# Kernel tuning notes

Hardware: AMD Instinct MI355X
Metric: run time of the kernel (lower is better)

Reference implementation:

```python
import jax, jax.numpy as jnp
import numpy as np

N = 100000      # nodes
E = 1600000     # edges (avg degree 16)
F_IN = 64
HID = 128
OUT = 64


def setup_inputs() -> dict:
    key = jax.random.key(0)
    ks = jax.random.split(key, 12)
    s = lambda k, i, o: jax.random.normal(k, (i, o), jnp.float32) / np.sqrt(i)
    x = jax.random.normal(ks[0], (N, F_IN), jnp.float32)
    edge_index = jax.random.randint(ks[1], (2, E), 0, N, dtype=jnp.int64)
    return {
        "x": x,
        "edge_index": edge_index,
        # conv1: SAGEConv(F_IN -> HID): lin_l (neighbors, with bias), lin_r (root)
        "W1n": s(ks[2], F_IN, HID), "b1n": jnp.zeros((HID,), jnp.float32),
        "W1r": s(ks[3], F_IN, HID),
        # lin1: Linear(F_IN -> HID)
        "Wl1": s(ks[4], F_IN, HID), "bl1": jnp.zeros((HID,), jnp.float32),
        # conv2: SAGEConv(HID -> OUT)
        "W2n": s(ks[5], HID, OUT), "b2n": jnp.zeros((OUT,), jnp.float32),
        "W2r": s(ks[6], HID, OUT),
        # lin2: Linear(HID -> OUT)
        "Wl2": s(ks[7], HID, OUT), "bl2": jnp.zeros((OUT,), jnp.float32),
    }


def _sage(x, src, dst, Wn, bn, Wr):
    # mean aggregation of source-node features at destination nodes
    msg = x[src]                                             # [E, F]
    agg = jax.ops.segment_sum(msg, dst, num_segments=N)      # [N, F]
    deg = jax.ops.segment_sum(jnp.ones((src.shape[0],), x.dtype), dst,
                              num_segments=N)                # [N]
    mean = agg / jnp.maximum(deg, 1.0)[:, None]
    return mean @ Wn + bn + x @ Wr


def reference(x, edge_index, W1n, b1n, W1r, Wl1, bl1, W2n, b2n, W2r, Wl2, bl2):
    src, dst = edge_index[0], edge_index[1]
    h = _sage(x, src, dst, W1n, b1n, W1r) + (x @ Wl1 + bl1)
    h = jax.nn.relu(h)
    out = _sage(h, src, dst, W2n, b2n, W2r) + (h @ Wl2 + bl2)
    return out
```

## Files before the change

kernel.cpp:

```cpp
#include <hip/hip_runtime.h>


#define NN 100000
#define NE 1600000
#define NSB 98
#define CAP2 18432
#define EPB 6250
#define MB 256
#define BSB 256
#define W1B 32
#define W2B 32
#define XBLK ((NN * 8 + 511) / 512)

typedef __attribute__((ext_vector_type(8))) __bf16 bf16x8;
typedef __attribute__((ext_vector_type(4))) float f32x4;

__device__ __forceinline__ float b2f(unsigned short u) {
    unsigned v = ((unsigned)u) << 16;
    float f;
    __builtin_memcpy(&f, &v, 4);
    return f;
}
__device__ __forceinline__ float b2f_lo(unsigned v) {
    unsigned w = v << 16;
    float f;
    __builtin_memcpy(&f, &w, 4);
    return f;
}
__device__ __forceinline__ float b2f_hi(unsigned v) {
    unsigned w = v & 0xFFFF0000u;
    float f;
    __builtin_memcpy(&f, &w, 4);
    return f;
}
__device__ __forceinline__ unsigned short f2b(float f) {
    unsigned u;
    __builtin_memcpy(&u, &f, 4);
    u += 0x7FFFu + ((u >> 16) & 1u);
    return (unsigned short)(u >> 16);
}

__global__ __launch_bounds__(512) void front_kernel(
    const void* __restrict__ x, const int* __restrict__ ei,
    const void* W1n, const void* W1r, const void* Wl1,
    const void* b1n, const void* bl1,
    const void* W2n, const void* W2r, const void* Wl2,
    const void* b2n, const void* bl2,
    unsigned short* __restrict__ Wt1g, unsigned short* __restrict__ Wt2g,
    float* __restrict__ bias1, float* __restrict__ bias2,
    unsigned int* __restrict__ xbu,
    int* __restrict__ flags, int* __restrict__ cntP, int* __restrict__ ebuf) {
    __shared__ int lh[NSB];
    __shared__ int lbase[NSB];
    __shared__ int ldst[EPB];
    __shared__ int sred[256];
    int t = threadIdx.x;
    int b = blockIdx.x;

    if (b < BSB) {
        if (t < 256) sred[t] = ei[2 * t + 1];
        if (t < NSB) lh[t] = 0;
        __syncthreads();
        for (int s = 128; s > 0; s >>= 1) {
            if (t < s) sred[t] |= sred[t + s];
            __syncthreads();
        }
        bool i64 = (sred[0] == 0);
        int e0 = b * EPB;
        for (int i = t; i < EPB; i += 512) {
            int e = e0 + i;
            int d = i64 ? (int)((const long long*)ei)[NE + e] : ei[NE + e];
            ldst[i] = d;
            atomicAdd(&lh[d >> 10], 1);
        }
        __syncthreads();
        if (t < NSB) {
            int c = lh[t];
            lbase[t] = c ? atomicAdd(&cntP[t * 16], c) : 0;
            lh[t] = 0;
        }
        __syncthreads();
        for (int i = t; i < EPB; i += 512) {
            int e = e0 + i;
            int s = i64 ? (int)((const long long*)ei)[e] : ei[e];
            int d = ldst[i];
            int sb = d >> 10;
            int r = lbase[sb] + atomicAdd(&lh[sb], 1);
            if (r < CAP2) ebuf[sb * CAP2 + r] = (s << 10) | (d & 1023);
        }
        return;
    }

    const unsigned int* xw = (const unsigned int*)x;
    if (t < 256) {
        unsigned e = (xw[t] >> 7) & 0xFFu;
        sred[t] = (e > 0x85u) ? 1 : 0;
    }
    __syncthreads();
    for (int s = 128; s > 0; s >>= 1) {
        if (t < s) sred[t] += sred[t + s];
        __syncthreads();
    }
    bool fp32 = sred[0] >= 32;
    auto rd = [&](const void* p, int i) -> float {
        return fp32 ? ((const float*)p)[i] : b2f(((const unsigned short*)p)[i]);
    };

    if (b < BSB + W1B) {
        int idx = (b - BSB) * 512 + t;
        int c = idx >> 7, k = idx & 127;
        float v = (k < 64) ? rd(W1n, k * 128 + c)
                           : rd(W1r, (k - 64) * 128 + c) + rd(Wl1, (k - 64) * 128 + c);
        Wt1g[c * 128 + k] = f2b(v);
        if (b == BSB) {
            if (t < 128) bias1[t] = rd(b1n, t) + rd(bl1, t);
            if (t == 0) flags[1] = fp32 ? 1 : 0;
        }
        return;
    }
    if (b < BSB + W1B + W2B) {
        int idx = (b - BSB - W1B) * 512 + t;
        int c = idx >> 7, k = idx & 127;
        float v = (c < 64) ? rd(W2n, k * 64 + c)
                           : rd(W2r, k * 64 + (c - 64)) + rd(Wl2, k * 64 + (c - 64));
        Wt2g[c * 128 + k] = f2b(v);
        if (b == BSB + W1B && t < 64) bias2[t] = rd(b2n, t) + rd(bl2, t);
        return;
    }
    int tt = (b - BSB - W1B - W2B) * 512 + t;
    if (tt >= NN * 8) return;
    if (fp32) {
        const float4* xf = (const float4*)x;
        float4 a = xf[2 * tt], c = xf[2 * tt + 1];
        uint4 o;
        o.x = f2b(a.x) | ((unsigned)f2b(a.y) << 16);
        o.y = f2b(a.z) | ((unsigned)f2b(a.w) << 16);
        o.z = f2b(c.x) | ((unsigned)f2b(c.y) << 16);
        o.w = f2b(c.z) | ((unsigned)f2b(c.w) << 16);
        ((uint4*)xbu)[tt] = o;
    } else {
        ((uint4*)xbu)[tt] = ((const uint4*)x)[tt];
    }
}

__global__ __launch_bounds__(512) void csr_build_kernel(
    const int* __restrict__ ebuf, const int* __restrict__ cntP,
    int* __restrict__ rpack, int* __restrict__ csr) {
    __shared__ int lcnt[1024];
    __shared__ int lsum[512];
    __shared__ int lcur[1024];
    int t = threadIdx.x, b = blockIdx.x;
    lcnt[t] = 0; lcnt[t + 512] = 0;
    __syncthreads();
    int base = b * CAP2;
    int cnt = min(cntP[b * 16], CAP2);
    for (int i = t; i < cnt; i += 512) atomicAdd(&lcnt[ebuf[base + i] & 1023], 1);
    __syncthreads();
    int c0 = lcnt[2 * t], c1 = lcnt[2 * t + 1];
    lsum[t] = c0 + c1;
    __syncthreads();
    for (int off = 1; off < 512; off <<= 1) {
        int v = lsum[t];
        int add = (t >= off) ? lsum[t - off] : 0;
        __syncthreads();
        lsum[t] = v + add;
        __syncthreads();
    }
    int excl = (t == 0) ? 0 : lsum[t - 1];
    int ex0 = excl, ex1 = excl + c0;
    lcur[2 * t] = ex0; lcur[2 * t + 1] = ex1;
    int d0 = b * 1024 + 2 * t;
    if (d0 < NN)     rpack[d0]     = ((base + ex0) << 8) | min(c0, 255);
    if (d0 + 1 < NN) rpack[d0 + 1] = ((base + ex1) << 8) | min(c1, 255);
    __syncthreads();
    for (int i = t; i < cnt; i += 512) {
        int pk = ebuf[base + i];
        int r = atomicAdd(&lcur[pk & 1023], 1);
        csr[base + r] = pk >> 10;
    }
}


__device__ __forceinline__ void gather_acc(
    const unsigned short* __restrict__ feat, const int* __restrict__ csr,
    int base, int deg, int fo, float* acc) {
    int t = 0;
    for (; t + 8 <= deg; t += 8) {
        int i0 = csr[base + t],     i1 = csr[base + t + 1];
        int i2 = csr[base + t + 2], i3 = csr[base + t + 3];
        int i4 = csr[base + t + 4], i5 = csr[base + t + 5];
        int i6 = csr[base + t + 6], i7 = csr[base + t + 7];
        bf16x8 v0 = *(const bf16x8*)(feat + (size_t)i0 * 64 + fo);
        bf16x8 v1 = *(const bf16x8*)(feat + (size_t)i1 * 64 + fo);
        bf16x8 v2 = *(const bf16x8*)(feat + (size_t)i2 * 64 + fo);
        bf16x8 v3 = *(const bf16x8*)(feat + (size_t)i3 * 64 + fo);
        bf16x8 v4 = *(const bf16x8*)(feat + (size_t)i4 * 64 + fo);
        bf16x8 v5 = *(const bf16x8*)(feat + (size_t)i5 * 64 + fo);
        bf16x8 v6 = *(const bf16x8*)(feat + (size_t)i6 * 64 + fo);
        bf16x8 v7 = *(const bf16x8*)(feat + (size_t)i7 * 64 + fo);
#pragma unroll
        for (int k = 0; k < 8; ++k)
            acc[k] += (((float)v0[k] + (float)v1[k]) + ((float)v2[k] + (float)v3[k]))
                    + (((float)v4[k] + (float)v5[k]) + ((float)v6[k] + (float)v7[k]));
    }
    for (; t + 4 <= deg; t += 4) {
        int i0 = csr[base + t],     i1 = csr[base + t + 1];
        int i2 = csr[base + t + 2], i3 = csr[base + t + 3];
        bf16x8 v0 = *(const bf16x8*)(feat + (size_t)i0 * 64 + fo);
        bf16x8 v1 = *(const bf16x8*)(feat + (size_t)i1 * 64 + fo);
        bf16x8 v2 = *(const bf16x8*)(feat + (size_t)i2 * 64 + fo);
        bf16x8 v3 = *(const bf16x8*)(feat + (size_t)i3 * 64 + fo);
#pragma unroll
        for (int k = 0; k < 8; ++k)
            acc[k] += ((float)v0[k] + (float)v1[k]) + ((float)v2[k] + (float)v3[k]);
    }
    for (; t < deg; ++t) {
        int i = csr[base + t];
        bf16x8 v = *(const bf16x8*)(feat + (size_t)i * 64 + fo);
#pragma unroll
        for (int k = 0; k < 8; ++k) acc[k] += (float)v[k];
    }
}

__global__ __launch_bounds__(256) void agg1_kernel(
    const unsigned short* __restrict__ feat, const int* __restrict__ rpack,
    const int* __restrict__ csr, unsigned int* __restrict__ mean1u) {
    int wid = threadIdx.x >> 6, lane = threadIdx.x & 63;
    int slot = lane >> 3, fo = (lane & 7) * 8;
    int d = (blockIdx.x * 4 + wid) * 8 + slot;
    int dd = min(d, NN - 1);
    int rp = rpack[dd];
    int base = rp >> 8;
    int deg = rp & 255;
    float acc[8];
#pragma unroll
    for (int k = 0; k < 8; ++k) acc[k] = 0.f;
    gather_acc(feat, csr, base, deg, fo, acc);
    if (d < NN) {
        float r = 1.0f / fmaxf((float)deg, 1.0f);
        uint4 o;
        o.x = f2b(acc[0] * r) | ((unsigned)f2b(acc[1] * r) << 16);
        o.y = f2b(acc[2] * r) | ((unsigned)f2b(acc[3] * r) << 16);
        o.z = f2b(acc[4] * r) | ((unsigned)f2b(acc[5] * r) << 16);
        o.w = f2b(acc[6] * r) | ((unsigned)f2b(acc[7] * r) << 16);
        *(uint4*)(mean1u + (size_t)d * 32 + (lane & 7) * 4) = o;
    }
}

__global__ __launch_bounds__(256) void agg2_kernel(
    const unsigned short* __restrict__ p, const int* __restrict__ rpack,
    const int* __restrict__ csr, const unsigned int* __restrict__ sfu,
    const float* __restrict__ bias2, const int* __restrict__ flags,
    void* __restrict__ out) {
    int wid = threadIdx.x >> 6, lane = threadIdx.x & 63;
    int slot = lane >> 3, fo = (lane & 7) * 8;
    int d = (blockIdx.x * 4 + wid) * 8 + slot;
    int dd = min(d, NN - 1);
    int rp = rpack[dd];
    int base = rp >> 8;
    int deg = rp & 255;
    float acc[8];
#pragma unroll
    for (int k = 0; k < 8; ++k) acc[k] = 0.f;
    gather_acc(p, csr, base, deg, fo, acc);
    if (d < NN) {
        float r = 1.0f / fmaxf((float)deg, 1.0f);
        uint4 sv = *(const uint4*)(sfu + (size_t)d * 32 + (lane & 7) * 4);
        float4 bA = *(const float4*)(bias2 + fo);
        float4 bB = *(const float4*)(bias2 + fo + 4);
        float v0 = acc[0] * r + b2f_lo(sv.x) + bA.x;
        float v1 = acc[1] * r + b2f_hi(sv.x) + bA.y;
        float v2 = acc[2] * r + b2f_lo(sv.y) + bA.z;
        float v3 = acc[3] * r + b2f_hi(sv.y) + bA.w;
        float v4 = acc[4] * r + b2f_lo(sv.z) + bB.x;
        float v5 = acc[5] * r + b2f_hi(sv.z) + bB.y;
        float v6 = acc[6] * r + b2f_lo(sv.w) + bB.z;
        float v7 = acc[7] * r + b2f_hi(sv.w) + bB.w;
        if (flags[1]) {
            float* op = (float*)out + (size_t)d * 64 + fo;
            *(float4*)op = make_float4(v0, v1, v2, v3);
            *(float4*)(op + 4) = make_float4(v4, v5, v6, v7);
        } else {
            uint4 o;
            o.x = f2b(v0) | ((unsigned)f2b(v1) << 16);
            o.y = f2b(v2) | ((unsigned)f2b(v3) << 16);
            o.z = f2b(v4) | ((unsigned)f2b(v5) << 16);
            o.w = f2b(v6) | ((unsigned)f2b(v7) << 16);
            *(uint4*)((unsigned int*)out + (size_t)d * 32 + (lane & 7) * 4) = o;
        }
    }
}

__global__ __launch_bounds__(512, 2) void gemmF_kernel(
    const unsigned short* __restrict__ mean1,
    const unsigned short* __restrict__ xb,
    const unsigned short* __restrict__ Wt1g, const float* __restrict__ bias1,
    const unsigned short* __restrict__ Wt2g,
    unsigned short* __restrict__ p, unsigned short* __restrict__ sf) {
    __shared__ unsigned short Wt1s[128 * 136];
    __shared__ unsigned short Wt2s[128 * 136];
    __shared__ unsigned short hs[MB * 136];
    int tid = threadIdx.x;
    int wid = tid >> 6, lane = tid & 63;
    int m = lane & 15, g = lane >> 4;
    int row0 = blockIdx.x * MB + wid * 32;

    bf16x8 a_frag[2][4];
#pragma unroll
    for (int t = 0; t < 2; ++t) {
        int arow = min(row0 + t * 16 + m, NN - 1);
#pragma unroll
        for (int kt = 0; kt < 4; ++kt) {
            int k0 = kt * 32 + g * 8;
            a_frag[t][kt] = (k0 < 64)
                ? *(const bf16x8*)(mean1 + (size_t)arow * 64 + k0)
                : *(const bf16x8*)(xb + (size_t)arow * 64 + (k0 - 64));
        }
    }

    for (int idx = tid; idx < 4096; idx += 512) {
        int c = (idx >> 4) & 127, ch = idx & 15;
        if (idx < 2048)
            *(bf16x8*)&Wt1s[c * 136 + ch * 8] = *(const bf16x8*)&Wt1g[c * 128 + ch * 8];
        else
            *(bf16x8*)&Wt2s[c * 136 + ch * 8] = *(const bf16x8*)&Wt2g[c * 128 + ch * 8];
    }
    __syncthreads();

    f32x4 acc[2][8];
#pragma unroll
    for (int t = 0; t < 2; ++t)
#pragma unroll
        for (int nt = 0; nt < 8; ++nt) acc[t][nt] = (f32x4){0.f, 0.f, 0.f, 0.f};

#pragma unroll
    for (int kt = 0; kt < 4; ++kt) {
        int k0 = kt * 32 + g * 8;
        bf16x8 b[8];
#pragma unroll
        for (int nt = 0; nt < 8; ++nt)
            b[nt] = *(const bf16x8*)(&Wt1s[(nt * 16 + m) * 136 + k0]);
#pragma unroll
        for (int nt = 0; nt < 8; ++nt) {
            acc[0][nt] = __builtin_amdgcn_mfma_f32_16x16x32_bf16(a_frag[0][kt], b[nt], acc[0][nt], 0, 0, 0);
            acc[1][nt] = __builtin_amdgcn_mfma_f32_16x16x32_bf16(a_frag[1][kt], b[nt], acc[1][nt], 0, 0, 0);
        }
    }

#pragma unroll
    for (int t = 0; t < 2; ++t)
#pragma unroll
        for (int nt = 0; nt < 8; ++nt) {
            int col = nt * 16 + m;
            float bias = bias1[col];
#pragma unroll
            for (int r = 0; r < 4; ++r) {
                float v = fmaxf(acc[t][nt][r] + bias, 0.0f);
                hs[(wid * 32 + t * 16 + g * 4 + r) * 136 + col] = f2b(v);
            }
        }

    bf16x8 a2[2][4];
#pragma unroll
    for (int t = 0; t < 2; ++t)
#pragma unroll
        for (int kt = 0; kt < 4; ++kt)
            a2[t][kt] = *(const bf16x8*)(&hs[(wid * 32 + t * 16 + m) * 136 + kt * 32 + g * 8]);

#pragma unroll
    for (int t = 0; t < 2; ++t)
#pragma unroll
        for (int nt = 0; nt < 8; ++nt) acc[t][nt] = (f32x4){0.f, 0.f, 0.f, 0.f};

#pragma unroll
    for (int kt = 0; kt < 4; ++kt) {
        int k0 = kt * 32 + g * 8;
        bf16x8 b[8];
#pragma unroll
        for (int nt = 0; nt < 8; ++nt)
            b[nt] = *(const bf16x8*)(&Wt2s[(nt * 16 + m) * 136 + k0]);
#pragma unroll
        for (int nt = 0; nt < 8; ++nt) {
            acc[0][nt] = __builtin_amdgcn_mfma_f32_16x16x32_bf16(a2[0][kt], b[nt], acc[0][nt], 0, 0, 0);
            acc[1][nt] = __builtin_amdgcn_mfma_f32_16x16x32_bf16(a2[1][kt], b[nt], acc[1][nt], 0, 0, 0);
        }
    }

#pragma unroll
    for (int t = 0; t < 2; ++t)
#pragma unroll
        for (int nt = 0; nt < 8; ++nt) {
            int col = nt * 16 + m;
#pragma unroll
            for (int r = 0; r < 4; ++r) {
                int row2 = row0 + t * 16 + g * 4 + r;
                if (row2 < NN) {
                    float v = acc[t][nt][r];
                    if (col < 64) p[(size_t)row2 * 64 + col] = f2b(v);
                    else          sf[(size_t)row2 * 64 + (col - 64)] = f2b(v);
                }
            }
        }
}

extern "C" void kernel_launch(void* const* d_in, const int* in_sizes, int n_in,
                              void* d_out, int out_size, void* d_ws, size_t ws_size,
                              hipStream_t stream) {
    const void* x   = d_in[0];
    const int*  ei  = (const int*)d_in[1];
    const void* W1n = d_in[2];
    const void* b1n = d_in[3];
    const void* W1r = d_in[4];
    const void* Wl1 = d_in[5];
    const void* bl1 = d_in[6];
    const void* W2n = d_in[7];
    const void* b2n = d_in[8];
    const void* W2r = d_in[9];
    const void* Wl2 = d_in[10];
    const void* bl2 = d_in[11];

    char* ws = (char*)d_ws;
    int*            flags = (int*)(ws + 0);
    int*            cntP  = (int*)(ws + 1024);
    int*            rpack = (int*)(ws + 8192);
    float*          bias1 = (float*)(ws + 409600);
    float*          bias2 = (float*)(ws + 410112);
    unsigned short* Wt1g  = (unsigned short*)(ws + 410368);
    unsigned short* Wt2g  = (unsigned short*)(ws + 443136);
    int*            csr   = (int*)(ws + 475904);
    unsigned short* xb    = (unsigned short*)(ws + 7701248);
    unsigned short* p     = xb;
    unsigned short* mean1 = (unsigned short*)(ws + 20501248);
    unsigned short* sf    = (unsigned short*)(ws + 33301248);
    int*            ebuf  = (int*)(ws + 46101248);

    (void)in_sizes; (void)n_in; (void)out_size; (void)ws_size;

    hipMemsetAsync(cntP, 0, NSB * 16 * sizeof(int), stream);
    front_kernel<<<BSB + W1B + W2B + XBLK, 512, 0, stream>>>(
        x, ei, W1n, W1r, Wl1, b1n, bl1, W2n, W2r, Wl2, b2n, bl2,
        Wt1g, Wt2g, bias1, bias2, (unsigned int*)xb, flags, cntP, ebuf);
    csr_build_kernel<<<NSB, 512, 0, stream>>>(ebuf, cntP, rpack, csr);
    agg1_kernel<<<(NN + 31) / 32, 256, 0, stream>>>(xb, rpack, csr, (unsigned int*)mean1);
    gemmF_kernel<<<(NN + MB - 1) / MB, 512, 0, stream>>>(mean1, xb, Wt1g, bias1, Wt2g, p, sf);
    agg2_kernel<<<(NN + 31) / 32, 256, 0, stream>>>(p, rpack, csr, (const unsigned int*)sf,
                                                    bias2, flags, d_out);
}
```

Measured before the change: 223.1 us.

## Replace two-pass bucketed CSR build with per-destination fixed-capacity adjacency slots

Edges are scattered straight into a padded per-destination array of 64 slots, claimed with a global atomic counter per node. This removes the coarse-bucket staging buffer and the whole CSR build kernel, along with its shared-memory histogram and scan. Both aggregation kernels now read the degree from the counter array and index the padded slots directly. The cost is a per-node counter memset, 1.6M global atomics and scattered 4-byte writes, and any node with more than 64 in-edges would silently lose edges.

```diff
diff --git a/kernel.cpp b/kernel.cpp
--- a/kernel.cpp
+++ b/kernel.cpp
@@ -3,11 +3,9 @@
 
 #define NN 100000
 #define NE 1600000
-#define NSB 98
-#define CAP2 18432
-#define EPB 6250
+#define CAPD 64
 #define MB 256
-#define BSB 256
+#define EB 3125
 #define W1B 32
 #define W2B 32
 #define XBLK ((NN * 8 + 511) / 512)
@@ -49,45 +47,25 @@
     unsigned short* __restrict__ Wt1g, unsigned short* __restrict__ Wt2g,
     float* __restrict__ bias1, float* __restrict__ bias2,
     unsigned int* __restrict__ xbu,
-    int* __restrict__ flags, int* __restrict__ cntP, int* __restrict__ ebuf) {
-    __shared__ int lh[NSB];
-    __shared__ int lbase[NSB];
-    __shared__ int ldst[EPB];
+    int* __restrict__ flags, int* __restrict__ cnt, int* __restrict__ csrD) {
     __shared__ int sred[256];
     int t = threadIdx.x;
     int b = blockIdx.x;
 
-    if (b < BSB) {
+    if (b < EB) {
         if (t < 256) sred[t] = ei[2 * t + 1];
-        if (t < NSB) lh[t] = 0;
         __syncthreads();
         for (int s = 128; s > 0; s >>= 1) {
             if (t < s) sred[t] |= sred[t + s];
             __syncthreads();
         }
         bool i64 = (sred[0] == 0);
-        int e0 = b * EPB;
-        for (int i = t; i < EPB; i += 512) {
-            int e = e0 + i;
-            int d = i64 ? (int)((const long long*)ei)[NE + e] : ei[NE + e];
-            ldst[i] = d;
-            atomicAdd(&lh[d >> 10], 1);
-        }
-        __syncthreads();
-        if (t < NSB) {
-            int c = lh[t];
-            lbase[t] = c ? atomicAdd(&cntP[t * 16], c) : 0;
-            lh[t] = 0;
-        }
-        __syncthreads();
-        for (int i = t; i < EPB; i += 512) {
-            int e = e0 + i;
-            int s = i64 ? (int)((const long long*)ei)[e] : ei[e];
-            int d = ldst[i];
-            int sb = d >> 10;
-            int r = lbase[sb] + atomicAdd(&lh[sb], 1);
-            if (r < CAP2) ebuf[sb * CAP2 + r] = (s << 10) | (d & 1023);
-        }
+        int e = b * 512 + t;
+        int s, d;
+        if (i64) { const long long* q = (const long long*)ei; s = (int)q[e]; d = (int)q[NE + e]; }
+        else     { s = ei[e]; d = ei[NE + e]; }
+        int r = atomicAdd(&cnt[d], 1);
+        if (r < CAPD) csrD[(size_t)d * CAPD + r] = s;
         return;
     }
 
@@ -106,28 +84,28 @@
         return fp32 ? ((const float*)p)[i] : b2f(((const unsigned short*)p)[i]);
     };
 
-    if (b < BSB + W1B) {
-        int idx = (b - BSB) * 512 + t;
+    if (b < EB + W1B) {
+        int idx = (b - EB) * 512 + t;
         int c = idx >> 7, k = idx & 127;
         float v = (k < 64) ? rd(W1n, k * 128 + c)
                            : rd(W1r, (k - 64) * 128 + c) + rd(Wl1, (k - 64) * 128 + c);
         Wt1g[c * 128 + k] = f2b(v);
-        if (b == BSB) {
+        if (b == EB) {
             if (t < 128) bias1[t] = rd(b1n, t) + rd(bl1, t);
             if (t == 0) flags[1] = fp32 ? 1 : 0;
         }
         return;
     }
-    if (b < BSB + W1B + W2B) {
-        int idx = (b - BSB - W1B) * 512 + t;
+    if (b < EB + W1B + W2B) {
+        int idx = (b - EB - W1B) * 512 + t;
         int c = idx >> 7, k = idx & 127;
         float v = (c < 64) ? rd(W2n, k * 64 + c)
                            : rd(W2r, k * 64 + (c - 64)) + rd(Wl2, k * 64 + (c - 64));
         Wt2g[c * 128 + k] = f2b(v);
-        if (b == BSB + W1B && t < 64) bias2[t] = rd(b2n, t) + rd(bl2, t);
+        if (b == EB + W1B && t < 64) bias2[t] = rd(b2n, t) + rd(bl2, t);
         return;
     }
-    int tt = (b - BSB - W1B - W2B) * 512 + t;
+    int tt = (b - EB - W1B - W2B) * 512 + t;
     if (tt >= NN * 8) return;
     if (fp32) {
         const float4* xf = (const float4*)x;
@@ -140,43 +118,6 @@
         ((uint4*)xbu)[tt] = o;
     } else {
         ((uint4*)xbu)[tt] = ((const uint4*)x)[tt];
-    }
-}
-
-__global__ __launch_bounds__(512) void csr_build_kernel(
-    const int* __restrict__ ebuf, const int* __restrict__ cntP,
-    int* __restrict__ rpack, int* __restrict__ csr) {
-    __shared__ int lcnt[1024];
-    __shared__ int lsum[512];
-    __shared__ int lcur[1024];
-    int t = threadIdx.x, b = blockIdx.x;
-    lcnt[t] = 0; lcnt[t + 512] = 0;
-    __syncthreads();
-    int base = b * CAP2;
-    int cnt = min(cntP[b * 16], CAP2);
-    for (int i = t; i < cnt; i += 512) atomicAdd(&lcnt[ebuf[base + i] & 1023], 1);
-    __syncthreads();
-    int c0 = lcnt[2 * t], c1 = lcnt[2 * t + 1];
-    lsum[t] = c0 + c1;
-    __syncthreads();
-    for (int off = 1; off < 512; off <<= 1) {
-        int v = lsum[t];
-        int add = (t >= off) ? lsum[t - off] : 0;
-        __syncthreads();
-        lsum[t] = v + add;
-        __syncthreads();
-    }
-    int excl = (t == 0) ? 0 : lsum[t - 1];
-    int ex0 = excl, ex1 = excl + c0;
-    lcur[2 * t] = ex0; lcur[2 * t + 1] = ex1;
-    int d0 = b * 1024 + 2 * t;
-    if (d0 < NN)     rpack[d0]     = ((base + ex0) << 8) | min(c0, 255);
-    if (d0 + 1 < NN) rpack[d0 + 1] = ((base + ex1) << 8) | min(c1, 255);
-    __syncthreads();
-    for (int i = t; i < cnt; i += 512) {
-        int pk = ebuf[base + i];
-        int r = atomicAdd(&lcur[pk & 1023], 1);
-        csr[base + r] = pk >> 10;
     }
 }
 
@@ -223,19 +164,18 @@
 }
 
 __global__ __launch_bounds__(256) void agg1_kernel(
-    const unsigned short* __restrict__ feat, const int* __restrict__ rpack,
-    const int* __restrict__ csr, unsigned int* __restrict__ mean1u) {
+    const unsigned short* __restrict__ feat, const int* __restrict__ cnt,
+    const int* __restrict__ csrD, unsigned int* __restrict__ mean1u) {
     int wid = threadIdx.x >> 6, lane = threadIdx.x & 63;
     int slot = lane >> 3, fo = (lane & 7) * 8;
     int d = (blockIdx.x * 4 + wid) * 8 + slot;
     int dd = min(d, NN - 1);
-    int rp = rpack[dd];
-    int base = rp >> 8;
-    int deg = rp & 255;
+    int deg = min(cnt[dd], CAPD);
+    int base = dd * CAPD;
     float acc[8];
 #pragma unroll
     for (int k = 0; k < 8; ++k) acc[k] = 0.f;
-    gather_acc(feat, csr, base, deg, fo, acc);
+    gather_acc(feat, csrD, base, deg, fo, acc);
     if (d < NN) {
         float r = 1.0f / fmaxf((float)deg, 1.0f);
         uint4 o;
@@ -248,21 +188,20 @@
 }
 
 __global__ __launch_bounds__(256) void agg2_kernel(
-    const unsigned short* __restrict__ p, const int* __restrict__ rpack,
-    const int* __restrict__ csr, const unsigned int* __restrict__ sfu,
+    const unsigned short* __restrict__ p, const int* __restrict__ cnt,
+    const int* __restrict__ csrD, const unsigned int* __restrict__ sfu,
     const float* __restrict__ bias2, const int* __restrict__ flags,
     void* __restrict__ out) {
     int wid = threadIdx.x >> 6, lane = threadIdx.x & 63;
     int slot = lane >> 3, fo = (lane & 7) * 8;
     int d = (blockIdx.x * 4 + wid) * 8 + slot;
     int dd = min(d, NN - 1);
-    int rp = rpack[dd];
-    int base = rp >> 8;
-    int deg = rp & 255;
+    int deg = min(cnt[dd], CAPD);
+    int base = dd * CAPD;
     float acc[8];
 #pragma unroll
     for (int k = 0; k < 8; ++k) acc[k] = 0.f;
-    gather_acc(p, csr, base, deg, fo, acc);
+    gather_acc(p, csrD, base, deg, fo, acc);
     if (d < NN) {
         float r = 1.0f / fmaxf((float)deg, 1.0f);
         uint4 sv = *(const uint4*)(sfu + (size_t)d * 32 + (lane & 7) * 4);
@@ -421,28 +360,25 @@
 
     char* ws = (char*)d_ws;
     int*            flags = (int*)(ws + 0);
-    int*            cntP  = (int*)(ws + 1024);
-    int*            rpack = (int*)(ws + 8192);
-    float*          bias1 = (float*)(ws + 409600);
-    float*          bias2 = (float*)(ws + 410112);
-    unsigned short* Wt1g  = (unsigned short*)(ws + 410368);
-    unsigned short* Wt2g  = (unsigned short*)(ws + 443136);
-    int*            csr   = (int*)(ws + 475904);
-    unsigned short* xb    = (unsigned short*)(ws + 7701248);
+    int*            cnt   = (int*)(ws + 1024);
+    float*          bias1 = (float*)(ws + 402432);
+    float*          bias2 = (float*)(ws + 402944);
+    unsigned short* Wt1g  = (unsigned short*)(ws + 403200);
+    unsigned short* Wt2g  = (unsigned short*)(ws + 435968);
+    int*            csrD  = (int*)(ws + 468736);
+    unsigned short* xb    = (unsigned short*)(ws + 26068736);
     unsigned short* p     = xb;
-    unsigned short* mean1 = (unsigned short*)(ws + 20501248);
-    unsigned short* sf    = (unsigned short*)(ws + 33301248);
-    int*            ebuf  = (int*)(ws + 46101248);
+    unsigned short* mean1 = (unsigned short*)(ws + 38868736);
+    unsigned short* sf    = (unsigned short*)(ws + 51668736);
 
     (void)in_sizes; (void)n_in; (void)out_size; (void)ws_size;
 
-    hipMemsetAsync(cntP, 0, NSB * 16 * sizeof(int), stream);
-    front_kernel<<<BSB + W1B + W2B + XBLK, 512, 0, stream>>>(
+    hipMemsetAsync(cnt, 0, NN * sizeof(int), stream);
+    front_kernel<<<EB + W1B + W2B + XBLK, 512, 0, stream>>>(
         x, ei, W1n, W1r, Wl1, b1n, bl1, W2n, W2r, Wl2, b2n, bl2,
-        Wt1g, Wt2g, bias1, bias2, (unsigned int*)xb, flags, cntP, ebuf);
-    csr_build_kernel<<<NSB, 512, 0, stream>>>(ebuf, cntP, rpack, csr);
-    agg1_kernel<<<(NN + 31) / 32, 256, 0, stream>>>(xb, rpack, csr, (unsigned int*)mean1);
+        Wt1g, Wt2g, bias1, bias2, (unsigned int*)xb, flags, cnt, csrD);
+    agg1_kernel<<<(NN + 31) / 32, 256, 0, stream>>>(xb, cnt, csrD, (unsigned int*)mean1);
     gemmF_kernel<<<(NN + MB - 1) / MB, 512, 0, stream>>>(mean1, xb, Wt1g, bias1, Wt2g, p, sf);
-    agg2_kernel<<<(NN + 31) / 32, 256, 0, stream>>>(p, rpack, csr, (const unsigned int*)sf,
+    agg2_kernel<<<(NN + 31) / 32, 256, 0, stream>>>(p, cnt, csrD, (const unsigned int*)sf,
                                                     bias2, flags, d_out);
 }
```

New measurement: 328.0 us. +47.0%, slower.
